# Performance work log

Hardware: AMD Instinct MI355X
Metric: run time of the kernel (lower is better)

The kernel has to match this reference:

```python
import jax, jax.numpy as jnp
import numpy as np

N_NODES = 30000
N_EDGES = 480000
B_PAIRS = 4096


def _lin(key, fan_in, fan_out):
    k1, k2 = jax.random.split(key)
    s = 1.0 / np.sqrt(fan_in)
    W = jax.random.uniform(k1, (fan_in, fan_out), minval=-s, maxval=s, dtype=jnp.float32)
    b = jax.random.uniform(k2, (fan_out,), minval=-s, maxval=s, dtype=jnp.float32)
    return W, b


def setup_inputs() -> dict:
    key = jax.random.key(0)
    ks = jax.random.split(key, 20)
    inp = {}
    inp["cid"] = jax.random.normal(ks[0], (N_NODES, 881), dtype=jnp.float32)
    inp["link_edge"] = jax.random.randint(ks[1], (2, N_EDGES), 0, N_NODES, dtype=jnp.int64)
    inp["i1"] = jax.random.randint(ks[2], (B_PAIRS,), 0, N_NODES, dtype=jnp.int64)
    inp["i2"] = jax.random.randint(ks[3], (B_PAIRS,), 0, N_NODES, dtype=jnp.int64)
    inp["soft_thr"] = jnp.array(0.01, jnp.float32)
    inp["bb_fc2_W"], inp["bb_fc2_b"] = _lin(ks[4], 881, 881)
    inp["bb_fc3_W"], inp["bb_fc3_b"] = _lin(ks[5], 881, 256)
    inp["gcn1_W"], inp["gcn1_b"] = _lin(ks[6], 256, 256)
    inp["gcn2_W"], inp["gcn2_b"] = _lin(ks[7], 256, 256)
    inp["gcn3_W"], inp["gcn3_b"] = _lin(ks[8], 256, 256)
    inp["gcn4_W"], inp["gcn4_b"] = _lin(ks[9], 256, 128)
    inp["gcn5_W"], inp["gcn5_b"] = _lin(ks[10], 128, 128)
    inp["fc1_W"], inp["fc1_b"] = _lin(ks[11], 256, 1024)
    inp["fc2_W"], inp["fc2_b"] = _lin(ks[12], 1024, 256)
    inp["fc3_W"], inp["fc3_b"] = _lin(ks[13], 256, 64)
    inp["out_W"], inp["out_b"] = _lin(ks[14], 64, 2)
    return inp


def _forward(cid, link_edge, i1, i2, soft_thr,
             bb_fc2_W, bb_fc2_b, bb_fc3_W, bb_fc3_b,
             gcn1_W, gcn1_b, gcn2_W, gcn2_b, gcn3_W, gcn3_b,
             gcn4_W, gcn4_b, gcn5_W, gcn5_b,
             fc1_W, fc1_b, fc2_W, fc2_b, fc3_W, fc3_b, out_W, out_b):
    N = cid.shape[0]
    # --- BasicBlock1 (eval mode, dropout off everywhere) ---
    x = jax.nn.relu(cid @ bb_fc2_W + bb_fc2_b)
    x = jnp.sign(x) * jax.nn.relu(jnp.abs(x) - soft_thr)  # soft threshold
    x = jax.nn.relu(x @ bb_fc3_W + bb_fc3_b)              # [N, 256]

    # --- GCN normalization (PyG GCNConv: add self-loops, sym norm) ---
    loop = jnp.arange(N, dtype=link_edge.dtype)
    src = jnp.concatenate([link_edge[0], loop])
    dst = jnp.concatenate([link_edge[1], loop])
    deg = jax.ops.segment_sum(jnp.ones_like(dst, dtype=jnp.float32), dst, num_segments=N)
    dinv = jnp.where(deg > 0, jax.lax.rsqrt(deg), 0.0)
    enorm = (dinv[src] * dinv[dst])[:, None]  # [E+N, 1]

    def gcn(h, W, b):
        h = h @ W                                            # [N, F_out]
        msg = h[src] * enorm                                 # gather + scale
        return jax.ops.segment_sum(msg, dst, num_segments=N) + b

    h = jax.nn.elu(gcn(x, gcn1_W, gcn1_b))
    h = jax.nn.elu(gcn(h, gcn2_W, gcn2_b))
    h = jax.nn.elu(gcn(h, gcn3_W, gcn3_b))
    h = jax.nn.elu(gcn(h, gcn4_W, gcn4_b))
    h = jax.nn.elu(gcn(h, gcn5_W, gcn5_b))                   # [N, 128]

    # --- pair readout ---
    xc = jnp.concatenate([h[i1], h[i2]], axis=1)             # [B, 256]
    norm = jnp.maximum(jnp.linalg.norm(xc, axis=1, keepdims=True), 1e-12)
    xc = xc / norm                                           # F.normalize(p=2, dim=1)
    xc = jax.nn.relu(xc @ fc1_W + fc1_b)
    xc = jax.nn.relu(xc @ fc2_W + fc2_b)
    xc = jax.nn.relu(xc @ fc3_W + fc3_b)
    return xc @ out_W + out_b                                # [B, 2]


def reference(cid, link_edge, i1, i2, soft_thr,
              bb_fc2_W, bb_fc2_b, bb_fc3_W, bb_fc3_b,
              gcn1_W, gcn1_b, gcn2_W, gcn2_b, gcn3_W, gcn3_b,
              gcn4_W, gcn4_b, gcn5_W, gcn5_b,
              fc1_W, fc1_b, fc2_W, fc2_b, fc3_W, fc3_b, out_W, out_b):
    return _forward(cid, link_edge, i1, i2, soft_thr,
                    bb_fc2_W, bb_fc2_b, bb_fc3_W, bb_fc3_b,
                    gcn1_W, gcn1_b, gcn2_W, gcn2_b, gcn3_W, gcn3_b,
                    gcn4_W, gcn4_b, gcn5_W, gcn5_b,
                    fc1_W, fc1_b, fc2_W, fc2_b, fc3_W, fc3_b, out_W, out_b)
```

## Files before the change

### kernel.cpp

```cpp
#include <hip/hip_runtime.h>
#include <hip/hip_bf16.h>
#include <math.h>


#define NNODES 30000
#define NEDGES 480000
#define NPAIRS 4096

typedef __attribute__((ext_vector_type(8))) short short8;
typedef __attribute__((ext_vector_type(4))) float f32x4;
typedef unsigned short u16;

__device__ __forceinline__ u16 f2bf(float x) {
    union { float f; unsigned u; } v; v.f = x;
    unsigned u = v.u;
    return (u16)((u + 0x7FFFu + ((u >> 16) & 1u)) >> 16);
}
__device__ __forceinline__ float bf2f(u16 h) {
    union { float f; unsigned u; } v; v.u = ((unsigned)h) << 16;
    return v.f;
}

__device__ __forceinline__ void gll16(const u16* g, u16* l) {
    __builtin_amdgcn_global_load_lds(
        (const __attribute__((address_space(1))) unsigned int*)g,
        (__attribute__((address_space(3))) unsigned int*)l, 16, 0, 0);
}


__global__ void k_count(const int* __restrict__ dst, unsigned* __restrict__ cnt, int E) {
    int e = blockIdx.x * blockDim.x + threadIdx.x;
    if (e < E) atomicAdd(&cnt[dst[e]], 1u);
}

__global__ void k_dinv(const unsigned* __restrict__ cnt, float* __restrict__ dinv, int N) {
    int n = blockIdx.x * blockDim.x + threadIdx.x;
    if (n < N) {
        float deg = (float)(cnt[n] + 1u);
        dinv[n] = 1.0f / sqrtf(deg);
    }
}

__global__ void k_scan1(const unsigned* __restrict__ cnt, unsigned* __restrict__ loc,
                        unsigned* __restrict__ part, int N) {
    __shared__ unsigned buf[256];
    int i = blockIdx.x * 256 + threadIdx.x;
    unsigned v = (i < N) ? cnt[i] : 0u;
    buf[threadIdx.x] = v;
    __syncthreads();
    for (int off = 1; off < 256; off <<= 1) {
        unsigned t = (threadIdx.x >= (unsigned)off) ? buf[threadIdx.x - off] : 0u;
        __syncthreads();
        buf[threadIdx.x] += t;
        __syncthreads();
    }
    if (i < N) loc[i] = buf[threadIdx.x];
    if (threadIdx.x == 255) part[blockIdx.x] = buf[255];
}

__global__ void k_scan2(unsigned* __restrict__ part, int nb) {
    if (threadIdx.x == 0 && blockIdx.x == 0) {
        unsigned s = 0;
        for (int i = 0; i < nb; ++i) { unsigned t = part[i]; part[i] = s; s += t; }
    }
}

__global__ void k_scan3(const unsigned* __restrict__ loc, const unsigned* __restrict__ part,
                        unsigned* __restrict__ rowptr, int N) {
    int i = blockIdx.x * 256 + threadIdx.x;
    if (i < N) rowptr[i + 1] = loc[i] + part[blockIdx.x];
    if (i == 0) rowptr[0] = 0;
}

__global__ void k_fill(const int* __restrict__ src, const int* __restrict__ dst,
                       const unsigned* __restrict__ rowptr, unsigned* __restrict__ cursor,
                       int* __restrict__ colsrc, int E) {
    int e = blockIdx.x * blockDim.x + threadIdx.x;
    if (e < E) {
        int d = dst[e];
        unsigned p = atomicAdd(&cursor[d], 1u);
        colsrc[rowptr[d] + p] = src[e];
    }
}


struct WJob { const float* W; u16* Th; u16* Tl; int K, N, Kp, Np, endBlk; };
struct WJobs { WJob j[10]; };

__global__ void k_wconv_all(WJobs js) {
    const int b = blockIdx.x;
    WJob jb = js.j[0];
    int blk0 = 0;
#pragma unroll
    for (int t = 1; t < 10; ++t)
        if (b >= js.j[t - 1].endBlk) { jb = js.j[t]; blk0 = js.j[t - 1].endBlk; }
    int idx = (b - blk0) * 256 + threadIdx.x;
    if (idx >= jb.Np * jb.Kp) return;
    int n = idx / jb.Kp, k = idx - n * jb.Kp;
    float v = (n < jb.N && k < jb.K) ? jb.W[(size_t)k * jb.N + n] : 0.f;
    u16 h = f2bf(v);
    jb.Th[idx] = h;
    jb.Tl[idx] = f2bf(v - bf2f(h));
}

__global__ void k_aconv(const float* __restrict__ A, u16* __restrict__ Hh,
                        u16* __restrict__ Hl) {
    int idx = blockIdx.x * blockDim.x + threadIdx.x;
    if (idx >= NNODES * 896) return;
    int row = idx / 896, col = idx - row * 896;
    float v = (col < 881) ? A[(size_t)row * 881 + col] : 0.f;
    u16 h = f2bf(v);
    Hh[idx] = h;
    Hl[idx] = f2bf(v - bf2f(h));
}


template <int ASRC, int EPI, int OUTM>
__global__ __launch_bounds__(256) void k_mgemm(
    const float* __restrict__ Af, int ldAf, int Ktrue,
    const u16* __restrict__ Ahi, const u16* __restrict__ Alo, int ldA,
    const u16* __restrict__ Bhi, const u16* __restrict__ Blo, int ldB,
    const float* __restrict__ bias, const float* __restrict__ thrp,
    const float* __restrict__ rowscale,
    float* __restrict__ Cf, u16* __restrict__ Chi, u16* __restrict__ Clo,
    int ldC, int M, int Ntrue, int K, int gy) {
    __shared__ alignas(16) u16 Ah[128 * 32];
    __shared__ alignas(16) u16 Al[128 * 32];
    __shared__ alignas(16) u16 Bh[128 * 32];
    __shared__ alignas(16) u16 Bl[128 * 32];
    const int t = threadIdx.x;
    const int lane = t & 63, w = t >> 6;
    const int wr = w >> 1, wc = w & 1;
    const int r16 = lane & 15, kg = lane >> 4;
    const int nwg = gridDim.x;
    const int q = nwg >> 3, r = nwg & 7;
    const int xcd = blockIdx.x & 7, pos = blockIdx.x >> 3;
    const int wg = (xcd < r ? xcd * (q + 1) : r * (q + 1) + (xcd - r) * q) + pos;
    const int bx = wg / gy, by = wg - bx * gy;
    const int bm = bx * 128, bn = by * 128;
    const int srow = (w << 5) + (lane >> 2);
    const int k8 = (lane & 3) << 3;
    const int lb = w << 11;
    f32x4 acc[4][4] = {};

    const int arow = t >> 1, kq = (t & 1) << 4;
    int gmA = bm + arow; if (gmA >= M) gmA = M - 1;
    const float* aBase = (ASRC == 0) ? (Af + (size_t)gmA * ldAf) : nullptr;
    float aR[16];

    auto LOADA = [&](int k0) {
#pragma unroll
        for (int j = 0; j < 16; ++j) aR[j] = aBase[k0 + kq + j];
    };
    auto WRITEA = [&](int k0) {
        short8 hv0, lv0, hv1, lv1;
#pragma unroll
        for (int j = 0; j < 8; ++j) {
            float v = (k0 + kq + j < Ktrue) ? aR[j] : 0.f;
            u16 hh = f2bf(v);
            hv0[j] = (short)hh;
            lv0[j] = (short)f2bf(v - bf2f(hh));
        }
#pragma unroll
        for (int j = 0; j < 8; ++j) {
            float v = (k0 + kq + 8 + j < Ktrue) ? aR[8 + j] : 0.f;
            u16 hh = f2bf(v);
            hv1[j] = (short)hh;
            lv1[j] = (short)f2bf(v - bf2f(hh));
        }
        const int wa = arow * 32 + kq;
        *(short8*)&Ah[wa] = hv0;  *(short8*)&Ah[wa + 8] = hv1;
        *(short8*)&Al[wa] = lv0;  *(short8*)&Al[wa + 8] = lv1;
    };

    if (ASRC == 0) LOADA(0);
    for (int k0 = 0; k0 < K; k0 += 32) {
        gll16(Bhi + (size_t)(bn + srow) * ldB + k0 + k8, (u16*)((char*)Bh + lb));
        gll16(Bhi + (size_t)(bn + srow + 16) * ldB + k0 + k8, (u16*)((char*)Bh + lb + 1024));
        gll16(Blo + (size_t)(bn + srow) * ldB + k0 + k8, (u16*)((char*)Bl + lb));
        gll16(Blo + (size_t)(bn + srow + 16) * ldB + k0 + k8, (u16*)((char*)Bl + lb + 1024));
        if (ASRC == 0) {
            WRITEA(k0);
        } else {
            gll16(Ahi + (size_t)(bm + srow) * ldA + k0 + k8, (u16*)((char*)Ah + lb));
            gll16(Ahi + (size_t)(bm + srow + 16) * ldA + k0 + k8, (u16*)((char*)Ah + lb + 1024));
            gll16(Alo + (size_t)(bm + srow) * ldA + k0 + k8, (u16*)((char*)Al + lb));
            gll16(Alo + (size_t)(bm + srow + 16) * ldA + k0 + k8, (u16*)((char*)Al + lb + 1024));
        }
        __syncthreads();
        if (ASRC == 0 && k0 + 32 < K) LOADA(k0 + 32);
        short8 fah[4], fal[4];
#pragma unroll
        for (int mi = 0; mi < 4; ++mi) {
            const int off = (wr * 64 + mi * 16 + r16) * 32 + kg * 8;
            fah[mi] = *(const short8*)&Ah[off];
            fal[mi] = *(const short8*)&Al[off];
        }
#pragma unroll
        for (int ni = 0; ni < 4; ++ni) {
            const int off = (wc * 64 + ni * 16 + r16) * 32 + kg * 8;
            const short8 fbh = *(const short8*)&Bh[off];
            const short8 fbl = *(const short8*)&Bl[off];
#pragma unroll
            for (int mi = 0; mi < 4; ++mi) {
                acc[mi][ni] = __builtin_amdgcn_mfma_f32_16x16x32_bf16(fah[mi], fbh, acc[mi][ni], 0, 0, 0);
                acc[mi][ni] = __builtin_amdgcn_mfma_f32_16x16x32_bf16(fal[mi], fbh, acc[mi][ni], 0, 0, 0);
                acc[mi][ni] = __builtin_amdgcn_mfma_f32_16x16x32_bf16(fah[mi], fbl, acc[mi][ni], 0, 0, 0);
            }
        }
        __syncthreads();
    }

    const float thr = (EPI == 2) ? *thrp : 0.f;
#pragma unroll
    for (int mi = 0; mi < 4; ++mi) {
#pragma unroll
        for (int i = 0; i < 4; ++i) {
            const int m = bm + wr * 64 + mi * 16 + kg * 4 + i;
            if (m >= M) continue;
            const float rs = (OUTM == 2) ? rowscale[m] : 1.f;
#pragma unroll
            for (int ni = 0; ni < 4; ++ni) {
                const int n = bn + wc * 64 + ni * 16 + r16;
                float z = acc[mi][ni][i];
                if (EPI >= 1) {
                    z += (n < Ntrue) ? bias[n] : 0.f;
                    z = (EPI == 1) ? fmaxf(z, 0.f) : fmaxf(z - thr, 0.f);
                }
                if (OUTM == 0) {
                    if (n < Ntrue) Cf[(size_t)m * ldC + n] = z;
                } else if (OUTM == 2) {
                    if (n < Ntrue) Cf[(size_t)m * ldC + n] = z * rs;
                } else {
                    if (n < ldC) {
                        if (n >= Ntrue) z = 0.f;
                        u16 h = f2bf(z);
                        size_t o = (size_t)m * ldC + n;
                        Chi[o] = h;
                        Clo[o] = f2bf(z - bf2f(h));
                    }
                }
            }
        }
    }
}


template <int NS, int WB>
__global__ __launch_bounds__(256) void k_aggs(
    const float* __restrict__ hWs, const float* __restrict__ dinv,
    const unsigned* __restrict__ rowptr, const int* __restrict__ colsrc,
    const float* __restrict__ bias, float* __restrict__ outf,
    u16* __restrict__ oh, u16* __restrict__ ol, int N) {
    const int F = NS * 32;
    const int m = blockIdx.x & 7;
    const int g = blockIdx.x >> 3;
    const int slice = (NS == 8) ? m : (m & 3);
    const int nbase = (NS == 8) ? (g << 3) : ((g << 4) + ((m >> 2) << 3));
    const int wave = threadIdx.x >> 6;
    const int half = (threadIdx.x >> 5) & 1;
    const int ln = threadIdx.x & 31;
    const int n = nbase + (wave << 1) + half;
    if (n >= N) return;
    const int fb = (slice << 5) + ln;
    const float* __restrict__ hb = hWs + fb;
    float acc = hb[(size_t)n * F];
    unsigned idx = rowptr[n];
    const unsigned end = rowptr[n + 1];
    for (; idx + 4 <= end; idx += 4) {
        int s0 = colsrc[idx], s1 = colsrc[idx + 1];
        int s2 = colsrc[idx + 2], s3 = colsrc[idx + 3];
        float a0 = hb[(size_t)s0 * F], a1 = hb[(size_t)s1 * F];
        float a2 = hb[(size_t)s2 * F], a3 = hb[(size_t)s3 * F];
        acc += (a0 + a1) + (a2 + a3);
    }
    for (; idx < end; ++idx) acc += hb[(size_t)colsrc[idx] * F];
    float z = dinv[n] * acc + bias[fb];
    z = (z > 0.f) ? z : expm1f(z);
    const size_t o = (size_t)n * F + fb;
    if (WB) {
        u16 h = f2bf(z);
        oh[o] = h;
        ol[o] = f2bf(z - bf2f(h));
    } else {
        outf[o] = z;
    }
}


__global__ __launch_bounds__(256) void k_pairs(
    const float* __restrict__ h, const int* __restrict__ i1, const int* __restrict__ i2,
    u16* __restrict__ xh, u16* __restrict__ xl, int B) {
    const int wave = threadIdx.x >> 6;
    const int lane = threadIdx.x & 63;
    const int p = blockIdx.x * 4 + wave;
    if (p >= B) return;
    const int a = i1[p], b = i2[p];
    float v0 = h[(size_t)a * 128 + lane];
    float v1 = h[(size_t)a * 128 + 64 + lane];
    float v2 = h[(size_t)b * 128 + lane];
    float v3 = h[(size_t)b * 128 + 64 + lane];
    float ss = v0 * v0 + v1 * v1 + v2 * v2 + v3 * v3;
#pragma unroll
    for (int o = 32; o > 0; o >>= 1) ss += __shfl_xor(ss, o, 64);
    float scale = 1.0f / fmaxf(sqrtf(ss), 1e-12f);
    size_t o = (size_t)p * 256;
    float vv[4] = {v0 * scale, v1 * scale, v2 * scale, v3 * scale};
#pragma unroll
    for (int j = 0; j < 4; ++j) {
        u16 hh = f2bf(vv[j]);
        xh[o + j * 64 + lane] = hh;
        xl[o + j * 64 + lane] = f2bf(vv[j] - bf2f(hh));
    }
}

__global__ __launch_bounds__(256) void k_out(
    const float* __restrict__ x, const float* __restrict__ W, const float* __restrict__ b,
    float* __restrict__ out, int B) {
    const int wave = threadIdx.x >> 6;
    const int lane = threadIdx.x & 63;
    const int p = blockIdx.x * 4 + wave;
    if (p >= B) return;
    float v = x[(size_t)p * 64 + lane];
    float s0 = v * W[lane * 2 + 0];
    float s1 = v * W[lane * 2 + 1];
#pragma unroll
    for (int o = 32; o > 0; o >>= 1) {
        s0 += __shfl_xor(s0, o, 64);
        s1 += __shfl_xor(s1, o, 64);
    }
    if (lane == 0) {
        out[p * 2 + 0] = s0 + b[0];
        out[p * 2 + 1] = s1 + b[1];
    }
}


extern "C" void kernel_launch(void* const* d_in, const int* in_sizes, int n_in,
                              void* d_out, int out_size, void* d_ws, size_t ws_size,
                              hipStream_t stream) {
    const float* cid = (const float*)d_in[0];
    const int* le   = (const int*)d_in[1];
    const int* i1   = (const int*)d_in[2];
    const int* i2   = (const int*)d_in[3];
    const float* thr = (const float*)d_in[4];
    const float* W2 = (const float*)d_in[5];  const float* b2 = (const float*)d_in[6];
    const float* W3 = (const float*)d_in[7];  const float* b3 = (const float*)d_in[8];
    const float* gW[5] = {(const float*)d_in[9],  (const float*)d_in[11], (const float*)d_in[13],
                          (const float*)d_in[15], (const float*)d_in[17]};
    const float* gB[5] = {(const float*)d_in[10], (const float*)d_in[12], (const float*)d_in[14],
                          (const float*)d_in[16], (const float*)d_in[18]};
    const float* fc1W = (const float*)d_in[19]; const float* fc1b = (const float*)d_in[20];
    const float* fc2W = (const float*)d_in[21]; const float* fc2b = (const float*)d_in[22];
    const float* fc3W = (const float*)d_in[23]; const float* fc3b = (const float*)d_in[24];
    const float* oW   = (const float*)d_in[25]; const float* ob   = (const float*)d_in[26];

    const int N = NNODES, E = NEDGES, B = NPAIRS;
    char* ws = (char*)d_ws;
    const bool big = ws_size >= 230000000ull;

    unsigned* cnt    = (unsigned*)(ws + 0);
    unsigned* cursor = (unsigned*)(ws + 120064);
    unsigned* rowptr = (unsigned*)(ws + 240128);
    int*      colsrc = (int*)     (ws + 360192);
    unsigned* loc    = (unsigned*)(ws + 360192);
    unsigned* part   = (unsigned*)(ws + 360192 + 122880);
    float*    dinv   = (float*)   (ws + 2280192);
    u16* W2th = (u16*)(ws + 2400256);  u16* W2tl = (u16*)(ws + 4005888);
    u16* W3th = (u16*)(ws + 5611520);  u16* W3tl = (u16*)(ws + 6070272);
    u16* g1h  = (u16*)(ws + 6529024);  u16* g1l  = (u16*)(ws + 6660096);
    u16* g2h  = (u16*)(ws + 6791168);  u16* g2l  = (u16*)(ws + 6922240);
    u16* g3h  = (u16*)(ws + 7053312);  u16* g3l  = (u16*)(ws + 7184384);
    u16* g4h  = (u16*)(ws + 7315456);  u16* g4l  = (u16*)(ws + 7380992);
    u16* g5h  = (u16*)(ws + 7446528);  u16* g5l  = (u16*)(ws + 7479296);
    u16* f1h  = (u16*)(ws + 7512064);  u16* f1l  = (u16*)(ws + 8036352);
    u16* f2h  = (u16*)(ws + 8560640);  u16* f2l  = (u16*)(ws + 9084928);
    u16* f3h  = (u16*)(ws + 9609216);  u16* f3l  = (u16*)(ws + 9674752);

    u16 *cidh = nullptr, *cidl = nullptr;
    u16 *x1h, *x1l, *x2h, *x2l, *hAh, *hAl, *xch, *xcl, *t1h, *t1l, *t2h, *t2l;
    float *hWs, *hfin, *t3;
    if (big) {
        const size_t CB = 9740288;
        const size_t XB = CB + 2ull * 53903360;
        cidh = (u16*)(ws + CB);
        cidl = (u16*)(ws + CB + 53903360);
        x1h  = (u16*)(ws + XB);
        x1l  = (u16*)(ws + XB + 53903360);
        x2h  = (u16*)(ws + CB);
        x2l  = (u16*)(ws + CB + 15400960);
        hWs  = (float*)(ws + CB + 30801920);
        hfin = (float*)(ws + CB + 61603840);
        xch  = (u16*)(ws + CB + 76963840);
        xcl  = (u16*)(ws + CB + 79060992);
        t1h  = (u16*)(ws + CB + 81158144);
        t1l  = (u16*)(ws + CB + 89546752);
        t2h  = (u16*)(ws + CB + 97935360);
        t2l  = (u16*)(ws + CB + 100032512);
        t3   = (float*)(ws + CB + 102129664);
        hAh  = (u16*)(ws + XB);
        hAl  = (u16*)(ws + XB + 15400960);
    } else {
        const size_t X1 = 40542208;
        x2h = (u16*)(ws + 9740288);
        x2l = (u16*)(ws + 25141248);
        x1h = (u16*)(ws + X1);
        x1l = (u16*)(ws + X1 + 53903360);
        hWs  = (float*)(ws + X1);
        hAh  = (u16*)  (ws + X1 + 30801920);
        hAl  = (u16*)  (ws + X1 + 46202880);
        hfin = (float*)(ws + X1 + 61603840);
        xch  = (u16*)  (ws + X1 + 76963840);
        xcl  = (u16*)  (ws + X1 + 79060992);
        t1h  = (u16*)  (ws + X1 + 81158144);
        t1l  = (u16*)  (ws + X1 + 89546752);
        t2h  = (u16*)  (ws + X1 + 97935360);
        t2l  = (u16*)  (ws + X1 + 100032512);
        t3   = (float*)(ws + X1 + 102129664);
    }

    hipMemsetAsync(cnt, 0, N * sizeof(unsigned), stream);
    hipMemsetAsync(cursor, 0, N * sizeof(unsigned), stream);
    k_count<<<(E + 255) / 256, 256, 0, stream>>>(le + E, cnt, E);
    k_dinv<<<(N + 255) / 256, 256, 0, stream>>>(cnt, dinv, N);
    const int NB = (N + 255) / 256;
    k_scan1<<<NB, 256, 0, stream>>>(cnt, loc, part, N);
    k_scan2<<<1, 64, 0, stream>>>(part, NB);
    k_scan3<<<NB, 256, 0, stream>>>(loc, part, rowptr, N);
    k_fill<<<(E + 255) / 256, 256, 0, stream>>>(le, le + E, rowptr, cursor, colsrc, E);

    {
        WJobs js;
        int e = 0;
        auto set = [&](int i, const float* W, u16* Th, u16* Tl, int K, int Nn, int Kp, int Np) {
            e += (Np * Kp) / 256;
            js.j[i] = WJob{W, Th, Tl, K, Nn, Kp, Np, e};
        };
        set(0, W2, W2th, W2tl, 881, 881, 896, 896);
        set(1, W3, W3th, W3tl, 881, 256, 896, 256);
        set(2, gW[0], g1h, g1l, 256, 256, 256, 256);
        set(3, gW[1], g2h, g2l, 256, 256, 256, 256);
        set(4, gW[2], g3h, g3l, 256, 256, 256, 256);
        set(5, gW[3], g4h, g4l, 256, 128, 256, 128);
        set(6, gW[4], g5h, g5l, 128, 128, 128, 128);
        set(7, fc1W, f1h, f1l, 256, 1024, 256, 1024);
        set(8, fc2W, f2h, f2l, 1024, 256, 1024, 256);
        set(9, fc3W, f3h, f3l, 256, 64, 256, 128);
        k_wconv_all<<<e, 256, 0, stream>>>(js);
    }

    const int MB = (N + 127) / 128;

    if (big) {
        k_aconv<<<(NNODES * 896 + 255) / 256, 256, 0, stream>>>(cid, cidh, cidl);
        k_mgemm<1, 2, 1><<<MB * 7, 256, 0, stream>>>(
            nullptr, 0, 0, cidh, cidl, 896, W2th, W2tl, 896, b2, thr, nullptr,
            nullptr, x1h, x1l, 896, N, 881, 896, 7);
    } else {
        k_mgemm<0, 2, 1><<<MB * 7, 256, 0, stream>>>(
            cid, 881, 881, nullptr, nullptr, 0, W2th, W2tl, 896, b2, thr, nullptr,
            nullptr, x1h, x1l, 896, N, 881, 896, 7);
    }
    k_mgemm<1, 1, 1><<<MB * 2, 256, 0, stream>>>(
        nullptr, 0, 0, x1h, x1l, 896, W3th, W3tl, 896, b3, nullptr, nullptr,
        nullptr, x2h, x2l, 256, N, 256, 896, 2);

    const u16* wh[5] = {g1h, g2h, g3h, g4h, g5h};
    const u16* wl[5] = {g1l, g2l, g3l, g4l, g5l};
    const int fin[5]  = {256, 256, 256, 256, 128};
    const int fout[5] = {256, 256, 256, 128, 128};
    u16* curh = x2h;  u16* curl = x2l;
    for (int l = 0; l < 5; ++l) {
        const int gy = fout[l] / 128;
        k_mgemm<1, 0, 2><<<MB * gy, 256, 0, stream>>>(
            nullptr, 0, 0, curh, curl, fin[l], wh[l], wl[l], fin[l], nullptr, nullptr, dinv,
            hWs, nullptr, nullptr, fout[l], N, fout[l], fin[l], gy);
        if (l == 4) {
            k_aggs<4, 0><<<8 * ((N + 15) / 16), 256, 0, stream>>>(
                hWs, dinv, rowptr, colsrc, gB[l], hfin, nullptr, nullptr, N);
        } else if (fout[l] == 256) {
            u16* oh = (l & 1) ? x2h : hAh;
            u16* ol = (l & 1) ? x2l : hAl;
            k_aggs<8, 1><<<8 * ((N + 7) / 8), 256, 0, stream>>>(
                hWs, dinv, rowptr, colsrc, gB[l], nullptr, oh, ol, N);
            curh = oh; curl = ol;
        } else {
            k_aggs<4, 1><<<8 * ((N + 15) / 16), 256, 0, stream>>>(
                hWs, dinv, rowptr, colsrc, gB[l], nullptr, x2h, x2l, N);
            curh = x2h; curl = x2l;
        }
    }

    k_pairs<<<(B + 3) / 4, 256, 0, stream>>>(hfin, i1, i2, xch, xcl, B);
    k_mgemm<1, 1, 1><<<32 * 8, 256, 0, stream>>>(
        nullptr, 0, 0, xch, xcl, 256, f1h, f1l, 256, fc1b, nullptr, nullptr,
        nullptr, t1h, t1l, 1024, B, 1024, 256, 8);
    k_mgemm<1, 1, 1><<<32 * 2, 256, 0, stream>>>(
        nullptr, 0, 0, t1h, t1l, 1024, f2h, f2l, 1024, fc2b, nullptr, nullptr,
        nullptr, t2h, t2l, 256, B, 256, 1024, 2);
    k_mgemm<1, 1, 0><<<32 * 1, 256, 0, stream>>>(
        nullptr, 0, 0, t2h, t2l, 256, f3h, f3l, 256, fc3b, nullptr, nullptr,
        t3, nullptr, nullptr, 64, B, 64, 256, 1);
    k_out<<<(B + 3) / 4, 256, 0, stream>>>(t3, oW, ob, (float*)d_out, B);
}
```

Measured before the change: 1.179 ms.

## Double-buffer GEMM LDS staging and use persistent atomic-queue GCN aggregation

GEMMs that read pre-split bf16 hi/lo operands now double-buffer their LDS tiles, issuing async global-to-LDS loads for the next K step while computing the current one. The fp32-input GEMM variant is split into its own kernel. GCN neighbour aggregation becomes a persistent kernel: a fixed grid of blocks pulls 16-node work items from per-slice atomic counters, and the slice order is rotated by XCC id to improve L2 locality per die. This adds LDS pressure, which can lower occupancy, plus atomic contention and a counter reset memset.

```diff
diff --git a/kernel.cpp b/kernel.cpp
--- a/kernel.cpp
+++ b/kernel.cpp
@@ -115,19 +115,15 @@
 }
 
 
-template <int ASRC, int EPI, int OUTM>
-__global__ __launch_bounds__(256) void k_mgemm(
-    const float* __restrict__ Af, int ldAf, int Ktrue,
+template <int EPI, int OUTM>
+__global__ __launch_bounds__(256) void k_mgemm2(
     const u16* __restrict__ Ahi, const u16* __restrict__ Alo, int ldA,
     const u16* __restrict__ Bhi, const u16* __restrict__ Blo, int ldB,
     const float* __restrict__ bias, const float* __restrict__ thrp,
     const float* __restrict__ rowscale,
     float* __restrict__ Cf, u16* __restrict__ Chi, u16* __restrict__ Clo,
     int ldC, int M, int Ntrue, int K, int gy) {
-    __shared__ alignas(16) u16 Ah[128 * 32];
-    __shared__ alignas(16) u16 Al[128 * 32];
-    __shared__ alignas(16) u16 Bh[128 * 32];
-    __shared__ alignas(16) u16 Bl[128 * 32];
+    __shared__ alignas(16) u16 lds[2][4][4096];
     const int t = threadIdx.x;
     const int lane = t & 63, w = t >> 6;
     const int wr = w >> 1, wc = w & 1;
@@ -140,67 +136,42 @@
     const int bm = bx * 128, bn = by * 128;
     const int srow = (w << 5) + (lane >> 2);
     const int k8 = (lane & 3) << 3;
-    const int lb = w << 11;
+    const int lbB = w << 11;
     f32x4 acc[4][4] = {};
 
-    const int arow = t >> 1, kq = (t & 1) << 4;
-    int gmA = bm + arow; if (gmA >= M) gmA = M - 1;
-    const float* aBase = (ASRC == 0) ? (Af + (size_t)gmA * ldAf) : nullptr;
-    float aR[16];
-
-    auto LOADA = [&](int k0) {
-#pragma unroll
-        for (int j = 0; j < 16; ++j) aR[j] = aBase[k0 + kq + j];
+    auto STAGE = [&](int buf, int k0) {
+        char* a0 = (char*)&lds[buf][0][0] + lbB;
+        char* a1 = (char*)&lds[buf][1][0] + lbB;
+        char* b0 = (char*)&lds[buf][2][0] + lbB;
+        char* b1 = (char*)&lds[buf][3][0] + lbB;
+        gll16(Ahi + (size_t)(bm + srow) * ldA + k0 + k8, (u16*)a0);
+        gll16(Ahi + (size_t)(bm + srow + 16) * ldA + k0 + k8, (u16*)(a0 + 1024));
+        gll16(Alo + (size_t)(bm + srow) * ldA + k0 + k8, (u16*)a1);
+        gll16(Alo + (size_t)(bm + srow + 16) * ldA + k0 + k8, (u16*)(a1 + 1024));
+        gll16(Bhi + (size_t)(bn + srow) * ldB + k0 + k8, (u16*)b0);
+        gll16(Bhi + (size_t)(bn + srow + 16) * ldB + k0 + k8, (u16*)(b0 + 1024));
+        gll16(Blo + (size_t)(bn + srow) * ldB + k0 + k8, (u16*)b1);
+        gll16(Blo + (size_t)(bn + srow + 16) * ldB + k0 + k8, (u16*)(b1 + 1024));
     };
-    auto WRITEA = [&](int k0) {
-        short8 hv0, lv0, hv1, lv1;
-#pragma unroll
-        for (int j = 0; j < 8; ++j) {
-            float v = (k0 + kq + j < Ktrue) ? aR[j] : 0.f;
-            u16 hh = f2bf(v);
-            hv0[j] = (short)hh;
-            lv0[j] = (short)f2bf(v - bf2f(hh));
-        }
-#pragma unroll
-        for (int j = 0; j < 8; ++j) {
-            float v = (k0 + kq + 8 + j < Ktrue) ? aR[8 + j] : 0.f;
-            u16 hh = f2bf(v);
-            hv1[j] = (short)hh;
-            lv1[j] = (short)f2bf(v - bf2f(hh));
-        }
-        const int wa = arow * 32 + kq;
-        *(short8*)&Ah[wa] = hv0;  *(short8*)&Ah[wa + 8] = hv1;
-        *(short8*)&Al[wa] = lv0;  *(short8*)&Al[wa + 8] = lv1;
-    };
-
-    if (ASRC == 0) LOADA(0);
-    for (int k0 = 0; k0 < K; k0 += 32) {
-        gll16(Bhi + (size_t)(bn + srow) * ldB + k0 + k8, (u16*)((char*)Bh + lb));
-        gll16(Bhi + (size_t)(bn + srow + 16) * ldB + k0 + k8, (u16*)((char*)Bh + lb + 1024));
-        gll16(Blo + (size_t)(bn + srow) * ldB + k0 + k8, (u16*)((char*)Bl + lb));
-        gll16(Blo + (size_t)(bn + srow + 16) * ldB + k0 + k8, (u16*)((char*)Bl + lb + 1024));
-        if (ASRC == 0) {
-            WRITEA(k0);
-        } else {
-            gll16(Ahi + (size_t)(bm + srow) * ldA + k0 + k8, (u16*)((char*)Ah + lb));
-            gll16(Ahi + (size_t)(bm + srow + 16) * ldA + k0 + k8, (u16*)((char*)Ah + lb + 1024));
-            gll16(Alo + (size_t)(bm + srow) * ldA + k0 + k8, (u16*)((char*)Al + lb));
-            gll16(Alo + (size_t)(bm + srow + 16) * ldA + k0 + k8, (u16*)((char*)Al + lb + 1024));
-        }
-        __syncthreads();
-        if (ASRC == 0 && k0 + 32 < K) LOADA(k0 + 32);
+
+    const int nk = K >> 5;
+    STAGE(0, 0);
+    __syncthreads();
+    int buf = 0;
+    for (int tt = 0; tt < nk; ++tt) {
+        if (tt + 1 < nk) STAGE(buf ^ 1, (tt + 1) << 5);
         short8 fah[4], fal[4];
 #pragma unroll
         for (int mi = 0; mi < 4; ++mi) {
             const int off = (wr * 64 + mi * 16 + r16) * 32 + kg * 8;
-            fah[mi] = *(const short8*)&Ah[off];
-            fal[mi] = *(const short8*)&Al[off];
+            fah[mi] = *(const short8*)&lds[buf][0][off];
+            fal[mi] = *(const short8*)&lds[buf][1][off];
         }
 #pragma unroll
         for (int ni = 0; ni < 4; ++ni) {
             const int off = (wc * 64 + ni * 16 + r16) * 32 + kg * 8;
-            const short8 fbh = *(const short8*)&Bh[off];
-            const short8 fbl = *(const short8*)&Bl[off];
+            const short8 fbh = *(const short8*)&lds[buf][2][off];
+            const short8 fbl = *(const short8*)&lds[buf][3][off];
 #pragma unroll
             for (int mi = 0; mi < 4; ++mi) {
                 acc[mi][ni] = __builtin_amdgcn_mfma_f32_16x16x32_bf16(fah[mi], fbh, acc[mi][ni], 0, 0, 0);
@@ -209,6 +180,7 @@
             }
         }
         __syncthreads();
+        buf ^= 1;
     }
 
     const float thr = (EPI == 2) ? *thrp : 0.f;
@@ -246,44 +218,165 @@
 }
 
 
+__global__ __launch_bounds__(256) void k_mgemmF(
+    const float* __restrict__ Af, int ldAf, int Ktrue,
+    const u16* __restrict__ Bhi, const u16* __restrict__ Blo, int ldB,
+    const float* __restrict__ bias, const float* __restrict__ thrp,
+    u16* __restrict__ Chi, u16* __restrict__ Clo,
+    int ldC, int M, int Ntrue, int K, int gy) {
+    __shared__ alignas(16) u16 Ah[128 * 32];
+    __shared__ alignas(16) u16 Al[128 * 32];
+    __shared__ alignas(16) u16 Bh[128 * 32];
+    __shared__ alignas(16) u16 Bl[128 * 32];
+    const int t = threadIdx.x;
+    const int lane = t & 63, w = t >> 6;
+    const int wr = w >> 1, wc = w & 1;
+    const int r16 = lane & 15, kg = lane >> 4;
+    const int nwg = gridDim.x;
+    const int q = nwg >> 3, r = nwg & 7;
+    const int xcd = blockIdx.x & 7, pos = blockIdx.x >> 3;
+    const int wg = (xcd < r ? xcd * (q + 1) : r * (q + 1) + (xcd - r) * q) + pos;
+    const int bx = wg / gy, by = wg - bx * gy;
+    const int bm = bx * 128, bn = by * 128;
+    const int srow = (w << 5) + (lane >> 2);
+    const int k8 = (lane & 3) << 3;
+    const int lb = w << 11;
+    f32x4 acc[4][4] = {};
+    const int arow = t >> 1, kq = (t & 1) << 4;
+    int gmA = bm + arow; if (gmA >= M) gmA = M - 1;
+    const float* aBase = Af + (size_t)gmA * ldAf;
+    float aR[16];
+#pragma unroll
+    for (int j = 0; j < 16; ++j) aR[j] = aBase[kq + j];
+    for (int k0 = 0; k0 < K; k0 += 32) {
+        gll16(Bhi + (size_t)(bn + srow) * ldB + k0 + k8, (u16*)((char*)Bh + lb));
+        gll16(Bhi + (size_t)(bn + srow + 16) * ldB + k0 + k8, (u16*)((char*)Bh + lb + 1024));
+        gll16(Blo + (size_t)(bn + srow) * ldB + k0 + k8, (u16*)((char*)Bl + lb));
+        gll16(Blo + (size_t)(bn + srow + 16) * ldB + k0 + k8, (u16*)((char*)Bl + lb + 1024));
+        {
+            short8 hv0, lv0, hv1, lv1;
+#pragma unroll
+            for (int j = 0; j < 8; ++j) {
+                float v = (k0 + kq + j < Ktrue) ? aR[j] : 0.f;
+                u16 hh = f2bf(v);
+                hv0[j] = (short)hh;
+                lv0[j] = (short)f2bf(v - bf2f(hh));
+            }
+#pragma unroll
+            for (int j = 0; j < 8; ++j) {
+                float v = (k0 + kq + 8 + j < Ktrue) ? aR[8 + j] : 0.f;
+                u16 hh = f2bf(v);
+                hv1[j] = (short)hh;
+                lv1[j] = (short)f2bf(v - bf2f(hh));
+            }
+            const int wa = arow * 32 + kq;
+            *(short8*)&Ah[wa] = hv0;  *(short8*)&Ah[wa + 8] = hv1;
+            *(short8*)&Al[wa] = lv0;  *(short8*)&Al[wa + 8] = lv1;
+        }
+        __syncthreads();
+        if (k0 + 32 < K) {
+#pragma unroll
+            for (int j = 0; j < 16; ++j) aR[j] = aBase[k0 + 32 + kq + j];
+        }
+        short8 fah[4], fal[4];
+#pragma unroll
+        for (int mi = 0; mi < 4; ++mi) {
+            const int off = (wr * 64 + mi * 16 + r16) * 32 + kg * 8;
+            fah[mi] = *(const short8*)&Ah[off];
+            fal[mi] = *(const short8*)&Al[off];
+        }
+#pragma unroll
+        for (int ni = 0; ni < 4; ++ni) {
+            const int off = (wc * 64 + ni * 16 + r16) * 32 + kg * 8;
+            const short8 fbh = *(const short8*)&Bh[off];
+            const short8 fbl = *(const short8*)&Bl[off];
+#pragma unroll
+            for (int mi = 0; mi < 4; ++mi) {
+                acc[mi][ni] = __builtin_amdgcn_mfma_f32_16x16x32_bf16(fah[mi], fbh, acc[mi][ni], 0, 0, 0);
+                acc[mi][ni] = __builtin_amdgcn_mfma_f32_16x16x32_bf16(fal[mi], fbh, acc[mi][ni], 0, 0, 0);
+                acc[mi][ni] = __builtin_amdgcn_mfma_f32_16x16x32_bf16(fah[mi], fbl, acc[mi][ni], 0, 0, 0);
+            }
+        }
+        __syncthreads();
+    }
+    const float thr = *thrp;
+#pragma unroll
+    for (int mi = 0; mi < 4; ++mi) {
+#pragma unroll
+        for (int i = 0; i < 4; ++i) {
+            const int m = bm + wr * 64 + mi * 16 + kg * 4 + i;
+            if (m >= M) continue;
+#pragma unroll
+            for (int ni = 0; ni < 4; ++ni) {
+                const int n = bn + wc * 64 + ni * 16 + r16;
+                float z = acc[mi][ni][i];
+                z += (n < Ntrue) ? bias[n] : 0.f;
+                z = fmaxf(z - thr, 0.f);
+                if (n < ldC) {
+                    if (n >= Ntrue) z = 0.f;
+                    u16 h = f2bf(z);
+                    size_t o = (size_t)m * ldC + n;
+                    Chi[o] = h;
+                    Clo[o] = f2bf(z - bf2f(h));
+                }
+            }
+        }
+    }
+}
+
+
 template <int NS, int WB>
-__global__ __launch_bounds__(256) void k_aggs(
+__global__ __launch_bounds__(256) void k_aggx(
     const float* __restrict__ hWs, const float* __restrict__ dinv,
     const unsigned* __restrict__ rowptr, const int* __restrict__ colsrc,
     const float* __restrict__ bias, float* __restrict__ outf,
-    u16* __restrict__ oh, u16* __restrict__ ol, int N) {
+    u16* __restrict__ oh, u16* __restrict__ ol,
+    unsigned* __restrict__ qq, int N) {
+    unsigned xcc;
+    asm volatile("s_getreg_b32 %0, hwreg(HW_REG_XCC_ID)" : "=s"(xcc));
     const int F = NS * 32;
-    const int m = blockIdx.x & 7;
-    const int g = blockIdx.x >> 3;
-    const int slice = (NS == 8) ? m : (m & 3);
-    const int nbase = (NS == 8) ? (g << 3) : ((g << 4) + ((m >> 2) << 3));
-    const int wave = threadIdx.x >> 6;
+    const int nslice = (NS == 8) ? 8 : 4;
     const int half = (threadIdx.x >> 5) & 1;
     const int ln = threadIdx.x & 31;
-    const int n = nbase + (wave << 1) + half;
-    if (n >= N) return;
-    const int fb = (slice << 5) + ln;
-    const float* __restrict__ hb = hWs + fb;
-    float acc = hb[(size_t)n * F];
-    unsigned idx = rowptr[n];
-    const unsigned end = rowptr[n + 1];
-    for (; idx + 4 <= end; idx += 4) {
-        int s0 = colsrc[idx], s1 = colsrc[idx + 1];
-        int s2 = colsrc[idx + 2], s3 = colsrc[idx + 3];
-        float a0 = hb[(size_t)s0 * F], a1 = hb[(size_t)s1 * F];
-        float a2 = hb[(size_t)s2 * F], a3 = hb[(size_t)s3 * F];
-        acc += (a0 + a1) + (a2 + a3);
-    }
-    for (; idx < end; ++idx) acc += hb[(size_t)colsrc[idx] * F];
-    float z = dinv[n] * acc + bias[fb];
-    z = (z > 0.f) ? z : expm1f(z);
-    const size_t o = (size_t)n * F + fb;
-    if (WB) {
-        u16 h = f2bf(z);
-        oh[o] = h;
-        ol[o] = f2bf(z - bf2f(h));
-    } else {
-        outf[o] = z;
+    const unsigned nitems = (unsigned)((N + 15) >> 4);
+    for (int so = 0; so < nslice; ++so) {
+        const int slice = ((int)xcc + so) & (nslice - 1);
+        const int fb = (slice << 5) + ln;
+        const float* __restrict__ hb = hWs + fb;
+        const float bsv = bias[fb];
+        for (;;) {
+            unsigned g;
+            if ((threadIdx.x & 63) == 0) g = atomicAdd(&qq[slice], 1u);
+            g = __shfl(g, 0, 64);
+            if (g >= nitems) break;
+            const int nb = (int)(g << 4);
+#pragma unroll 1
+            for (int i = 0; i < 8; ++i) {
+                const int n = nb + i * 2 + half;
+                if (n >= N) continue;
+                float acc = hb[(size_t)n * F];
+                unsigned idx = rowptr[n];
+                const unsigned end = rowptr[n + 1];
+                for (; idx + 4 <= end; idx += 4) {
+                    int s0 = colsrc[idx], s1 = colsrc[idx + 1];
+                    int s2 = colsrc[idx + 2], s3 = colsrc[idx + 3];
+                    float a0 = hb[(size_t)s0 * F], a1 = hb[(size_t)s1 * F];
+                    float a2 = hb[(size_t)s2 * F], a3 = hb[(size_t)s3 * F];
+                    acc += (a0 + a1) + (a2 + a3);
+                }
+                for (; idx < end; ++idx) acc += hb[(size_t)colsrc[idx] * F];
+                float z = dinv[n] * acc + bsv;
+                z = (z > 0.f) ? z : expm1f(z);
+                const size_t o = (size_t)n * F + fb;
+                if (WB) {
+                    u16 h = f2bf(z);
+                    oh[o] = h;
+                    ol[o] = f2bf(z - bf2f(h));
+                } else {
+                    outf[o] = z;
+                }
+            }
+        }
     }
 }
 
@@ -360,6 +453,7 @@
     const bool big = ws_size >= 230000000ull;
 
     unsigned* cnt    = (unsigned*)(ws + 0);
+    unsigned* aggq   = (unsigned*)(ws + 0);
     unsigned* cursor = (unsigned*)(ws + 120064);
     unsigned* rowptr = (unsigned*)(ws + 240128);
     int*      colsrc = (int*)     (ws + 360192);
@@ -428,6 +522,7 @@
     k_scan2<<<1, 64, 0, stream>>>(part, NB);
     k_scan3<<<NB, 256, 0, stream>>>(loc, part, rowptr, N);
     k_fill<<<(E + 255) / 256, 256, 0, stream>>>(le, le + E, rowptr, cursor, colsrc, E);
+    hipMemsetAsync(aggq, 0, 40 * sizeof(unsigned), stream);
 
     {
         WJobs js;
@@ -453,16 +548,16 @@
 
     if (big) {
         k_aconv<<<(NNODES * 896 + 255) / 256, 256, 0, stream>>>(cid, cidh, cidl);
-        k_mgemm<1, 2, 1><<<MB * 7, 256, 0, stream>>>(
-            nullptr, 0, 0, cidh, cidl, 896, W2th, W2tl, 896, b2, thr, nullptr,
+        k_mgemm2<2, 1><<<MB * 7, 256, 0, stream>>>(
+            cidh, cidl, 896, W2th, W2tl, 896, b2, thr, nullptr,
             nullptr, x1h, x1l, 896, N, 881, 896, 7);
     } else {
-        k_mgemm<0, 2, 1><<<MB * 7, 256, 0, stream>>>(
-            cid, 881, 881, nullptr, nullptr, 0, W2th, W2tl, 896, b2, thr, nullptr,
-            nullptr, x1h, x1l, 896, N, 881, 896, 7);
-    }
-    k_mgemm<1, 1, 1><<<MB * 2, 256, 0, stream>>>(
-        nullptr, 0, 0, x1h, x1l, 896, W3th, W3tl, 896, b3, nullptr, nullptr,
+        k_mgemmF<<<MB * 7, 256, 0, stream>>>(
+            cid, 881, 881, W2th, W2tl, 896, b2, thr,
+            x1h, x1l, 896, N, 881, 896, 7);
+    }
+    k_mgemm2<1, 1><<<MB * 2, 256, 0, stream>>>(
+        x1h, x1l, 896, W3th, W3tl, 896, b3, nullptr, nullptr,
         nullptr, x2h, x2l, 256, N, 256, 896, 2);
 
     const u16* wh[5] = {g1h, g2h, g3h, g4h, g5h};
@@ -472,34 +567,35 @@
     u16* curh = x2h;  u16* curl = x2l;
     for (int l = 0; l < 5; ++l) {
         const int gy = fout[l] / 128;
-        k_mgemm<1, 0, 2><<<MB * gy, 256, 0, stream>>>(
-            nullptr, 0, 0, curh, curl, fin[l], wh[l], wl[l], fin[l], nullptr, nullptr, dinv,
+        k_mgemm2<0, 2><<<MB * gy, 256, 0, stream>>>(
+            curh, curl, fin[l], wh[l], wl[l], fin[l], nullptr, nullptr, dinv,
             hWs, nullptr, nullptr, fout[l], N, fout[l], fin[l], gy);
+        unsigned* ql = aggq + l * 8;
         if (l == 4) {
-            k_aggs<4, 0><<<8 * ((N + 15) / 16), 256, 0, stream>>>(
-                hWs, dinv, rowptr, colsrc, gB[l], hfin, nullptr, nullptr, N);
+            k_aggx<4, 0><<<2048, 256, 0, stream>>>(
+                hWs, dinv, rowptr, colsrc, gB[l], hfin, nullptr, nullptr, ql, N);
         } else if (fout[l] == 256) {
             u16* oh = (l & 1) ? x2h : hAh;
             u16* ol = (l & 1) ? x2l : hAl;
-            k_aggs<8, 1><<<8 * ((N + 7) / 8), 256, 0, stream>>>(
-                hWs, dinv, rowptr, colsrc, gB[l], nullptr, oh, ol, N);
+            k_aggx<8, 1><<<2048, 256, 0, stream>>>(
+                hWs, dinv, rowptr, colsrc, gB[l], nullptr, oh, ol, ql, N);
             curh = oh; curl = ol;
         } else {
-            k_aggs<4, 1><<<8 * ((N + 15) / 16), 256, 0, stream>>>(
-                hWs, dinv, rowptr, colsrc, gB[l], nullptr, x2h, x2l, N);
+            k_aggx<4, 1><<<2048, 256, 0, stream>>>(
+                hWs, dinv, rowptr, colsrc, gB[l], nullptr, x2h, x2l, ql, N);
             curh = x2h; curl = x2l;
         }
     }
 
     k_pairs<<<(B + 3) / 4, 256, 0, stream>>>(hfin, i1, i2, xch, xcl, B);
-    k_mgemm<1, 1, 1><<<32 * 8, 256, 0, stream>>>(
-        nullptr, 0, 0, xch, xcl, 256, f1h, f1l, 256, fc1b, nullptr, nullptr,
+    k_mgemm2<1, 1><<<32 * 8, 256, 0, stream>>>(
+        xch, xcl, 256, f1h, f1l, 256, fc1b, nullptr, nullptr,
         nullptr, t1h, t1l, 1024, B, 1024, 256, 8);
-    k_mgemm<1, 1, 1><<<32 * 2, 256, 0, stream>>>(
-        nullptr, 0, 0, t1h, t1l, 1024, f2h, f2l, 1024, fc2b, nullptr, nullptr,
+    k_mgemm2<1, 1><<<32 * 2, 256, 0, stream>>>(
+        t1h, t1l, 1024, f2h, f2l, 1024, fc2b, nullptr, nullptr,
         nullptr, t2h, t2l, 256, B, 256, 1024, 2);
-    k_mgemm<1, 1, 0><<<32 * 1, 256, 0, stream>>>(
-        nullptr, 0, 0, t2h, t2l, 256, f3h, f3l, 256, fc3b, nullptr, nullptr,
+    k_mgemm2<1, 0><<<32 * 1, 256, 0, stream>>>(
+        t2h, t2l, 256, f3h, f3l, 256, fc3b, nullptr, nullptr,
         t3, nullptr, nullptr, 64, B, 64, 256, 1);
     k_out<<<(B + 3) / 4, 256, 0, stream>>>(t3, oW, ob, (float*)d_out, B);
 }
```

After: 4.604 ms. 3.9x slower.
